# Performance work log

Measured on AMD Instinct MI355X. Metric: run time of the kernel, lower is better.

## Reference

```python
import jax, jax.numpy as jnp
import numpy as np
from jax import lax

NMS_RADIUS = 4  # module default


def conv2d(x, w, b, pad):
    # x: [B,C,H,W], w: [O,I,kh,kw]
    y = lax.conv_general_dilated(x, w, window_strides=(1, 1),
                                 padding=[(pad, pad), (pad, pad)],
                                 dimension_numbers=('NCHW', 'OIHW', 'NCHW'))
    return y + b[None, :, None, None]


def max_pool(x, r):
    # x: [B,H,W]; kernel (2r+1)x(2r+1), stride 1, pad r (torch pads with -inf)
    k = 2 * r + 1
    return lax.reduce_window(x, -jnp.inf, lax.max,
                             window_dimensions=(1, k, k),
                             window_strides=(1, 1, 1),
                             padding=[(0, 0), (r, r), (r, r)])


def simple_nms(scores, r):
    zeros = jnp.zeros_like(scores)
    max_mask = scores == max_pool(scores, r)
    for _ in range(2):
        supp_mask = max_pool(max_mask.astype(scores.dtype), r) > 0
        supp_scores = jnp.where(supp_mask, zeros, scores)
        new_max_mask = supp_scores == max_pool(supp_scores, r)
        max_mask = max_mask | (new_max_mask & ~supp_mask)
    return jnp.where(max_mask, scores, zeros)


def setup_inputs() -> dict:
    key = jax.random.key(0)
    ks = jax.random.split(key, 7)
    B, Hc, Wc = 16, 60, 80
    x = jax.random.normal(ks[0], (B, 512, Hc, Wc), dtype=jnp.float32)
    wPa = jax.random.normal(ks[1], (256, 512, 3, 3), dtype=jnp.float32) * 0.02
    bPa = jax.random.normal(ks[2], (256,), dtype=jnp.float32) * 0.02
    wPd = jax.random.normal(ks[3], (128, 256, 3, 3), dtype=jnp.float32) * 0.02
    bPd = jax.random.normal(ks[4], (128,), dtype=jnp.float32) * 0.02
    wPg = jax.random.normal(ks[5], (65, 128, 1, 1), dtype=jnp.float32) * 0.02
    bPg = jax.random.normal(ks[6], (65,), dtype=jnp.float32) * 0.02
    return {'x': x, 'wPa': wPa, 'bPa': bPa, 'wPd': wPd, 'bPd': bPd,
            'wPg': wPg, 'bPg': bPg}


def reference(x, wPa, bPa, wPd, bPd, wPg, bPg):
    h1 = jax.nn.relu(conv2d(x, wPa, bPa, pad=1))          # [B,256,Hc,Wc]
    h2 = jax.nn.relu(conv2d(h1, wPd, bPd, pad=1))         # [B,128,Hc,Wc]
    logits = conv2d(h2, wPg, bPg, pad=0)                  # [B,65,Hc,Wc]
    scores = jax.nn.softmax(logits, axis=1)[:, :-1]       # [B,64,Hc,Wc]
    b, _, h, w = scores.shape
    # pixel-unshuffle 8x8 cells -> full resolution
    scores = scores.transpose(0, 2, 3, 1).reshape(b, h, w, 8, 8)
    scores = scores.transpose(0, 1, 3, 2, 4).reshape(b, h * 8, w * 8)
    return simple_nms(scores, NMS_RADIUS)
```

## Files before the change

### kernel.cpp

```cpp
#include <hip/hip_runtime.h>
#include <hip/hip_bf16.h>
#include <math.h>


#define B_      16
#define HC      60
#define WC      80
#define PIX     (HC * WC)
#define HF      480
#define WF      640
#define IMG     (HF * WF)
#define NPIX    (B_ * IMG)

typedef double f64x4 __attribute__((ext_vector_type(4)));

__device__ __forceinline__ int clampi(int v, int lo, int hi) {
    return v < lo ? lo : (v > hi ? hi : v);
}

__global__ __launch_bounds__(256) void cvt_f32_f64(const float* __restrict__ s,
                                                   double* __restrict__ d, int n)
{
    int i = blockIdx.x * 256 + threadIdx.x;
    if (i < n) d[i] = (double)s[i];
}

__global__ __launch_bounds__(256) void prep_w(const float* __restrict__ w,
                                              double* __restrict__ wT,
                                              int CIN, int n)
{
    int i = blockIdx.x * 256 + threadIdx.x;
    if (i >= n) return;
    int cin9 = CIN * 9;
    int oc   = i / cin9;
    int rem  = i - oc * cin9;
    int ic   = rem / 9;
    int dydx = rem - ic * 9;
    size_t dst = ((size_t)((oc >> 4) * (CIN >> 2) + (ic >> 2)) * 9 + dydx) * 64
               + (ic & 3) * 16 + (oc & 15);
    wT[dst] = (double)w[i];
}

template <int CIN, typename TIN, bool RELU>
__global__ __launch_bounds__(256, 3) void conv3x3_mfma(
    const TIN* __restrict__ in,
    const double* __restrict__ wT,
    const double* __restrict__ bias,
    double* __restrict__ out)
{
    const int COUT  = (CIN == 512) ? 256 : 128;
    const int NCH   = CIN / 4;
    const int ytile = blockIdx.x;
    const int ocq   = blockIdx.y;
    const int b     = blockIdx.z;
    const int tid   = threadIdx.x;
    const int wv    = tid >> 6;
    const int lane  = tid & 63;
    const int q     = lane >> 4;
    const int c     = lane & 15;
    const int wr    = wv & 1;
    const int wo    = wv >> 1;
    const int y0    = ytile * 2;
    const int y     = y0 + wr;

    in  += (size_t)b * CIN  * PIX;
    out += (size_t)b * COUT * PIX;

    int rowL[4], colL[4];
    {
        f64x4 pr = (f64x4){0.0, 0.0, 0.0, 0.0};
        double a1 = (lane < 16) ? (double)(16 * lane) : 0.0;
        double b1 = (lane < 16) ? 1.0 : 0.0;
        pr = __builtin_amdgcn_mfma_f64_16x16x4f64(a1, b1, pr, 0, 0, 0);
        double a2 = (lane < 16) ? 1.0 : 0.0;
        double b2 = (lane < 16) ? (double)lane : 0.0;
        pr = __builtin_amdgcn_mfma_f64_16x16x4f64(a2, b2, pr, 0, 0, 0);
#pragma unroll
        for (int i = 0; i < 4; ++i) {
            int code = (int)pr[i];
            rowL[i] = (code >> 4) & 15;
            colL[i] = code & 15;
        }
    }

    __shared__ double smem[2][1312];

    const int ocb0 = ocq * 4 + wo * 2;
    const double* wA = wT + (size_t)ocb0 * NCH * 576;
    const double* wB = wT + (size_t)(ocb0 + 1) * NCH * 576;

    f64x4 acc[2][5];
#pragma unroll
    for (int o = 0; o < 2; ++o)
#pragma unroll
        for (int t = 0; t < 5; ++t) acc[o][t] = (f64x4){0.0, 0.0, 0.0, 0.0};

    const int bbase = q * 328 + wr * 82 + c;

    int aOff[6];
#pragma unroll
    for (int j = 0; j < 6; ++j) {
        int i   = tid + j * 256;
        int ick = i / 328;
        int rem = i - ick * 328;
        int ry  = rem / 82;
        int rx  = rem - ry * 82;
        int gy  = y0 - 1 + ry, gx = rx - 1;
        bool ok = (i < 1312) && ((unsigned)gy < (unsigned)HC) && ((unsigned)gx < (unsigned)WC);
        aOff[j] = ok ? (ick * PIX + gy * WC + gx) : -1;
    }

    double ra[6];

#define LOADC(ch)                                                              \
    {                                                                          \
        const int gbase = (ch) * 4 * PIX;                                      \
        _Pragma("unroll")                                                      \
        for (int j = 0; j < 6; ++j)                                            \
            ra[j] = (aOff[j] >= 0) ? (double)in[gbase + aOff[j]] : 0.0;        \
    }

#define STOREC(sel)                                                            \
    {                                                                          \
        double* dst = smem[sel];                                               \
        _Pragma("unroll")                                                      \
        for (int j = 0; j < 5; ++j) dst[tid + j * 256] = ra[j];                \
        if (tid < 32) dst[1280 + tid] = ra[5];                                 \
    }

    LOADC(0);
    STOREC(0);
    LOADC(1);
    __syncthreads();

    for (int chk = 0; chk < NCH; ++chk) {
        const int cur = chk & 1;
        if (chk + 1 < NCH) STOREC(cur ^ 1);
        if (chk + 2 < NCH) LOADC(chk + 2);

        const double* wa  = wA + (size_t)chk * 576;
        const double* wb  = wB + (size_t)chk * 576;
        const double* act = smem[cur];

#pragma unroll
        for (int dy = 0; dy < 3; ++dy) {
#pragma unroll
            for (int dx = 0; dx < 3; ++dx) {
                const int d = dy * 3 + dx;
                double a0 = wa[d * 64 + lane];
                double a1 = wb[d * 64 + lane];
#pragma unroll
                for (int t = 0; t < 5; ++t) {
                    double bv = act[bbase + dy * 82 + t * 16 + dx];
                    acc[0][t] = __builtin_amdgcn_mfma_f64_16x16x4f64(a0, bv, acc[0][t], 0, 0, 0);
                    acc[1][t] = __builtin_amdgcn_mfma_f64_16x16x4f64(a1, bv, acc[1][t], 0, 0, 0);
                }
            }
        }
        if (chk + 1 < NCH) __syncthreads();
    }
#undef LOADC
#undef STOREC

#pragma unroll
    for (int o = 0; o < 2; ++o) {
#pragma unroll
        for (int t = 0; t < 5; ++t) {
#pragma unroll
            for (int i = 0; i < 4; ++i) {
                const int oc = (ocb0 + o) * 16 + rowL[i];
                double v = acc[o][t][i] + bias[oc];
                if (RELU) v = fmax(v, 0.0);
                out[(size_t)oc * PIX + y * WC + t * 16 + colL[i]] = v;
            }
        }
    }
}

__global__ __launch_bounds__(256) void conv1x1_softmax_f64(
    const double* __restrict__ h2,
    const double* __restrict__ wg,
    const double* __restrict__ bg,
    double* __restrict__ S)
{
    int p = blockIdx.x * 256 + threadIdx.x;
    if (p >= PIX) return;
    const int b = blockIdx.y;
    const double* h2p = h2 + (size_t)b * 128 * PIX + p;
    double* Sb = S + (size_t)b * IMG;

    double l[65];
#pragma unroll
    for (int o = 0; o < 65; ++o) l[o] = bg[o];

    for (int icc = 0; icc < 128; icc += 8) {
        double h[8];
#pragma unroll
        for (int k = 0; k < 8; ++k) h[k] = h2p[(size_t)(icc + k) * PIX];
#pragma unroll
        for (int o = 0; o < 65; ++o) {
            const double* wp = wg + o * 128 + icc;
            l[o] += h[0] * wp[0] + h[1] * wp[1] + h[2] * wp[2] + h[3] * wp[3]
                  + h[4] * wp[4] + h[5] * wp[5] + h[6] * wp[6] + h[7] * wp[7];
        }
    }

    double m = l[0];
#pragma unroll
    for (int o = 1; o < 65; ++o) m = fmax(m, l[o]);
    double s = 0.0;
#pragma unroll
    for (int o = 0; o < 65; ++o) { l[o] = exp(l[o] - m); s += l[o]; }
    double inv = 1.0 / s;

    int y = p / WC, x = p % WC;
#pragma unroll
    for (int cy = 0; cy < 8; ++cy)
#pragma unroll
        for (int cx2 = 0; cx2 < 8; ++cx2)
            Sb[(y * 8 + cy) * WF + x * 8 + cx2] = l[cy * 8 + cx2] * inv;
}

__global__ __launch_bounds__(256) void hmax9_f64(const double* __restrict__ in,
                                                 double* __restrict__ out)
{
    int p = blockIdx.x * 256 + threadIdx.x;
    int x = p % WF;
    const double* row = in + (p - x);
    double m = row[x];
#pragma unroll
    for (int d = 1; d <= 4; ++d) {
        m = fmax(m, row[clampi(x - d, 0, WF - 1)]);
        m = fmax(m, row[clampi(x + d, 0, WF - 1)]);
    }
    out[p] = m;
}

__global__ __launch_bounds__(256) void vmax9_eq(const double* __restrict__ T,
                                                const double* __restrict__ S,
                                                unsigned char* __restrict__ M)
{
    int p = blockIdx.x * 256 + threadIdx.x;
    int y = (p % IMG) / WF;
    double m = T[p];
#pragma unroll
    for (int d = 1; d <= 4; ++d) {
        m = fmax(m, T[p + (clampi(y - d, 0, HF - 1) - y) * WF]);
        m = fmax(m, T[p + (clampi(y + d, 0, HF - 1) - y) * WF]);
    }
    M[p] = (S[p] == m) ? (unsigned char)1 : (unsigned char)0;
}

__global__ __launch_bounds__(256) void hor9_u8(const unsigned char* __restrict__ in,
                                               unsigned char* __restrict__ out)
{
    int p = blockIdx.x * 256 + threadIdx.x;
    int x = p % WF;
    const unsigned char* row = in + (p - x);
    unsigned char m = row[x];
#pragma unroll
    for (int d = 1; d <= 4; ++d) {
        m = m | row[clampi(x - d, 0, WF - 1)];
        m = m | row[clampi(x + d, 0, WF - 1)];
    }
    out[p] = m;
}

__global__ __launch_bounds__(256) void vor9_sup(const unsigned char* __restrict__ T8,
                                                unsigned char* __restrict__ SUP)
{
    int p = blockIdx.x * 256 + threadIdx.x;
    int y = (p % IMG) / WF;
    unsigned char m = T8[p];
#pragma unroll
    for (int d = 1; d <= 4; ++d) {
        m = m | T8[p + (clampi(y - d, 0, HF - 1) - y) * WF];
        m = m | T8[p + (clampi(y + d, 0, HF - 1) - y) * WF];
    }
    SUP[p] = m;
}

__global__ __launch_bounds__(256) void hmax9_supp(const double* __restrict__ S,
                                                  const unsigned char* __restrict__ SUP,
                                                  double* __restrict__ T)
{
    int p = blockIdx.x * 256 + threadIdx.x;
    int x = p % WF;
    int base = p - x;
    double m = SUP[p] ? 0.0 : S[p];
#pragma unroll
    for (int d = 1; d <= 4; ++d) {
        int i1 = base + clampi(x - d, 0, WF - 1);
        int i2 = base + clampi(x + d, 0, WF - 1);
        m = fmax(m, SUP[i1] ? 0.0 : S[i1]);
        m = fmax(m, SUP[i2] ? 0.0 : S[i2]);
    }
    T[p] = m;
}

__global__ __launch_bounds__(256) void vmax9_newmask(const double* __restrict__ T,
                                                     const double* __restrict__ S,
                                                     const unsigned char* __restrict__ SUP,
                                                     unsigned char* __restrict__ M)
{
    int p = blockIdx.x * 256 + threadIdx.x;
    int y = (p % IMG) / WF;
    double m = T[p];
#pragma unroll
    for (int d = 1; d <= 4; ++d) {
        m = fmax(m, T[p + (clampi(y - d, 0, HF - 1) - y) * WF]);
        m = fmax(m, T[p + (clampi(y + d, 0, HF - 1) - y) * WF]);
    }
    unsigned char nw = (!SUP[p] && S[p] == m) ? 1 : 0;
    M[p] = M[p] | nw;
}

__global__ __launch_bounds__(256) void final_mask(const double* __restrict__ S,
                                                  const unsigned char* __restrict__ M,
                                                  float* __restrict__ out)
{
    int p = blockIdx.x * 256 + threadIdx.x;
    out[p] = M[p] ? (float)S[p] : 0.f;
}

extern "C" void kernel_launch(void* const* d_in, const int* in_sizes, int n_in,
                              void* d_out, int out_size, void* d_ws, size_t ws_size,
                              hipStream_t stream)
{
    const float* x   = (const float*)d_in[0];
    const float* wPa = (const float*)d_in[1];
    const float* bPa = (const float*)d_in[2];
    const float* wPd = (const float*)d_in[3];
    const float* bPd = (const float*)d_in[4];
    const float* wPg = (const float*)d_in[5];
    const float* bPg = (const float*)d_in[6];
    float* out = (float*)d_out;

    char* ws = (char*)d_ws;
    double*        S   = (double*)(ws);
    double*        T   = (double*)(ws + 39321600);
    unsigned char* M   = (unsigned char*)(ws + 78643200);
    unsigned char* SUP = (unsigned char*)(ws + 83558400);
    unsigned char* T8  = (unsigned char*)(ws + 88473600);
    double* w1t = (double*)(ws + 39321600);
    double* w2t = (double*)(ws + 48758784);
    double* wgd = (double*)(ws + 51118080);
    double* b1d = (double*)(ws + 51184640);
    double* b2d = (double*)(ws + 51186688);
    double* bgd = (double*)(ws + 51187712);
    char*   hbase = ws + 51188736;

    int G = 1;
    for (int g = 16; g >= 1; g >>= 1) {
        if ((size_t)51188736 + (size_t)g * 14745600 <= ws_size) { G = g; break; }
    }

    prep_w<<<(1179648 + 255) / 256, 256, 0, stream>>>(wPa, w1t, 512, 1179648);
    prep_w<<<(294912 + 255) / 256, 256, 0, stream>>>(wPd, w2t, 256, 294912);
    cvt_f32_f64<<<(8320 + 255) / 256, 256, 0, stream>>>(wPg, wgd, 8320);
    cvt_f32_f64<<<1, 256, 0, stream>>>(bPa, b1d, 256);
    cvt_f32_f64<<<1, 256, 0, stream>>>(bPd, b2d, 128);
    cvt_f32_f64<<<1, 256, 0, stream>>>(bPg, bgd, 65);

    for (int bg0 = 0; bg0 < B_; bg0 += G) {
        int Gc = (bg0 + G <= B_) ? G : (B_ - bg0);
        double* h1s = (double*)hbase;
        double* h2s = (double*)(hbase + (size_t)G * 9830400);
        const float* xb = x + (size_t)bg0 * 512 * PIX;
        conv3x3_mfma<512, float, true><<<dim3(30, 4, Gc), 256, 0, stream>>>(xb, w1t, b1d, h1s);
        conv3x3_mfma<256, double, true><<<dim3(30, 2, Gc), 256, 0, stream>>>(h1s, w2t, b2d, h2s);
        conv1x1_softmax_f64<<<dim3(19, Gc), 256, 0, stream>>>(h2s, wgd, bgd, S + (size_t)bg0 * IMG);
    }

    const int NB = NPIX / 256;
    hmax9_f64<<<NB, 256, 0, stream>>>(S, T);
    vmax9_eq<<<NB, 256, 0, stream>>>(T, S, M);
    for (int it = 0; it < 2; ++it) {
        hor9_u8<<<NB, 256, 0, stream>>>(M, T8);
        vor9_sup<<<NB, 256, 0, stream>>>(T8, SUP);
        hmax9_supp<<<NB, 256, 0, stream>>>(S, SUP, T);
        vmax9_newmask<<<NB, 256, 0, stream>>>(T, S, SUP, M);
    }
    final_mask<<<NB, 256, 0, stream>>>(S, M, out);
}
```

Before: 4.471 ms.

## Drop LDS staging in conv3x3 and read activations directly from global

Removes the double-buffered shared-memory tile and its barriers from the 3x3 MFMA convolution. Each lane now loads its input activations straight from global memory with per-element bounds checks, relying on L1/L2 caches to serve the overlapping 3x3 reuse. This eliminates the LDS stores and __syncthreads, but adds many more global loads (45 per chunk per lane instead of about 6) and exposes their latency without explicit prefetching.

```diff
diff --git a/kernel.cpp b/kernel.cpp
--- a/kernel.cpp
+++ b/kernel.cpp
@@ -60,8 +60,7 @@
     const int c     = lane & 15;
     const int wr    = wv & 1;
     const int wo    = wv >> 1;
-    const int y0    = ytile * 2;
-    const int y     = y0 + wr;
+    const int y     = ytile * 2 + wr;
 
     in  += (size_t)b * CIN  * PIX;
     out += (size_t)b * COUT * PIX;
@@ -83,8 +82,6 @@
         }
     }
 
-    __shared__ double smem[2][1312];
-
     const int ocb0 = ocq * 4 + wo * 2;
     const double* wA = wT + (size_t)ocb0 * NCH * 576;
     const double* wB = wT + (size_t)(ocb0 + 1) * NCH * 576;
@@ -95,55 +92,16 @@
 #pragma unroll
         for (int t = 0; t < 5; ++t) acc[o][t] = (f64x4){0.0, 0.0, 0.0, 0.0};
 
-    const int bbase = q * 328 + wr * 82 + c;
-
-    int aOff[6];
-#pragma unroll
-    for (int j = 0; j < 6; ++j) {
-        int i   = tid + j * 256;
-        int ick = i / 328;
-        int rem = i - ick * 328;
-        int ry  = rem / 82;
-        int rx  = rem - ry * 82;
-        int gy  = y0 - 1 + ry, gx = rx - 1;
-        bool ok = (i < 1312) && ((unsigned)gy < (unsigned)HC) && ((unsigned)gx < (unsigned)WC);
-        aOff[j] = ok ? (ick * PIX + gy * WC + gx) : -1;
-    }
-
-    double ra[6];
-
-#define LOADC(ch)                                                              \
-    {                                                                          \
-        const int gbase = (ch) * 4 * PIX;                                      \
-        _Pragma("unroll")                                                      \
-        for (int j = 0; j < 6; ++j)                                            \
-            ra[j] = (aOff[j] >= 0) ? (double)in[gbase + aOff[j]] : 0.0;        \
-    }
-
-#define STOREC(sel)                                                            \
-    {                                                                          \
-        double* dst = smem[sel];                                               \
-        _Pragma("unroll")                                                      \
-        for (int j = 0; j < 5; ++j) dst[tid + j * 256] = ra[j];                \
-        if (tid < 32) dst[1280 + tid] = ra[5];                                 \
-    }
-
-    LOADC(0);
-    STOREC(0);
-    LOADC(1);
-    __syncthreads();
-
     for (int chk = 0; chk < NCH; ++chk) {
-        const int cur = chk & 1;
-        if (chk + 1 < NCH) STOREC(cur ^ 1);
-        if (chk + 2 < NCH) LOADC(chk + 2);
-
-        const double* wa  = wA + (size_t)chk * 576;
-        const double* wb  = wB + (size_t)chk * 576;
-        const double* act = smem[cur];
+        const TIN* icp = in + (size_t)(chk * 4 + q) * PIX;
+        const double* wa = wA + (size_t)chk * 576;
+        const double* wb = wB + (size_t)chk * 576;
 
 #pragma unroll
         for (int dy = 0; dy < 3; ++dy) {
+            const int row = y + dy - 1;
+            const bool rowOK = (unsigned)row < (unsigned)HC;
+            const TIN* rp = icp + row * WC;
 #pragma unroll
             for (int dx = 0; dx < 3; ++dx) {
                 const int d = dy * 3 + dx;
@@ -151,16 +109,16 @@
                 double a1 = wb[d * 64 + lane];
 #pragma unroll
                 for (int t = 0; t < 5; ++t) {
-                    double bv = act[bbase + dy * 82 + t * 16 + dx];
+                    const int col = c - 1 + t * 16 + dx;
+                    double bv = 0.0;
+                    if (rowOK && (unsigned)col < (unsigned)WC)
+                        bv = (double)rp[col];
                     acc[0][t] = __builtin_amdgcn_mfma_f64_16x16x4f64(a0, bv, acc[0][t], 0, 0, 0);
                     acc[1][t] = __builtin_amdgcn_mfma_f64_16x16x4f64(a1, bv, acc[1][t], 0, 0, 0);
                 }
             }
         }
-        if (chk + 1 < NCH) __syncthreads();
-    }
-#undef LOADC
-#undef STOREC
+    }
 
 #pragma unroll
     for (int o = 0; o < 2; ++o) {
```

Result: slower. 5.613 ms (+25.5%).
